# Kernel optimization log

Measured on AMD Instinct MI355X. Metric: run time of the kernel, lower is better.

Reference implementation:

```python
import jax, jax.numpy as jnp
import numpy as np

N_EMBD = 768
HEAD_SIZE = 64
B, T = 8, 4096


def setup_inputs() -> dict:
    key = jax.random.key(0)
    ks = jax.random.split(key, 7)
    s = 0.02  # small init scale for weights
    return {
        "x": jax.random.normal(ks[0], (B, T, N_EMBD), dtype=jnp.float32),
        "Wq": jax.random.normal(ks[1], (N_EMBD, HEAD_SIZE), dtype=jnp.float32) * s,
        "bq": jax.random.normal(ks[2], (HEAD_SIZE,), dtype=jnp.float32) * s,
        "Wk": jax.random.normal(ks[3], (N_EMBD, HEAD_SIZE), dtype=jnp.float32) * s,
        "bk": jax.random.normal(ks[4], (HEAD_SIZE,), dtype=jnp.float32) * s,
        "Wv": jax.random.normal(ks[5], (N_EMBD, HEAD_SIZE), dtype=jnp.float32) * s,
        "bv": jax.random.normal(ks[6], (HEAD_SIZE,), dtype=jnp.float32) * s,
    }


def reference(x, Wq, bq, Wk, bk, Wv, bv):
    # x: [B, T, C]; note: scale uses C = n_embd (input dim), per the original code.
    C = x.shape[-1]
    scale = jnp.asarray(C, x.dtype) ** -0.5
    q = x @ Wq + bq  # [B, T, H]
    k = x @ Wk + bk  # [B, T, H]
    v = x @ Wv + bv  # [B, T, H]
    wei = jnp.einsum("bqh,bkh->bqk", q, k) * scale  # [B, T, T]
    att = jax.nn.softmax(wei, axis=-1)
    # dropout p=0.0 (eval mode) -> identity
    out = jnp.einsum("bqk,bkh->bqh", att, v)  # [B, T, H]
    return out
```

## Files before the change

### kernel.cpp

```cpp
#include <hip/hip_runtime.h>
#include <stdint.h>

#define T_SEQ 4096
#define CEMB 768
#define HS 64

typedef __attribute__((ext_vector_type(8))) short bf16x8;
typedef __attribute__((ext_vector_type(16))) float f32x16;
typedef __attribute__((ext_vector_type(4))) unsigned int u32x4;

__device__ __forceinline__ short bfru(float f) {
    uint32_t u = __builtin_bit_cast(uint32_t, f);
    return (short)((u + 0x8000u) >> 16);
}
__device__ __forceinline__ uint32_t cvtpk_bf16(float lo, float hi) {
    uint32_t r;
    asm("v_cvt_pk_bf16_f32 %0, %1, %2" : "=v"(r) : "v"(lo), "v"(hi));
    return r;
}

#define QSCALE (0.036084391824351615f * 1.4426950408889634f)

__global__ __launch_bounds__(256) void prep_wt(const float* __restrict__ Wq,
                                               const float* __restrict__ Wk,
                                               const float* __restrict__ Wv,
                                               short* __restrict__ wtf) {
    const int p = blockIdx.x;
    const int tid = threadIdx.x;
    const int lane = tid & 63, jp = tid >> 6;
    const int l31 = lane & 31, lhi = lane >> 5;
    const int kq = p % 48, ct = p / 48;
    const int k = kq * 16 + lhi * 8 + jp * 2;
    const int nn = ct * 32 + l31;
    const float* W = nn < 64 ? Wq : (nn < 128 ? Wk : Wv);
    const int col = nn & 63;
    uint32_t lo = (uint16_t)bfru(W[k * 64 + col]);
    uint32_t hi = (uint16_t)bfru(W[(k + 1) * 64 + col]);
    *(uint32_t*)&wtf[(p * 64 + lane) * 8 + jp * 2] = lo | (hi << 16);
}

__global__ __launch_bounds__(256, 4) void qkv_proj(const float* __restrict__ x,
        const float* __restrict__ bq, const float* __restrict__ bk, const float* __restrict__ bv,
        const short* __restrict__ wtf,
        short* __restrict__ qo, short* __restrict__ ko, short* __restrict__ vto) {
    __shared__ short S[2][32 * 72];

    const int tid  = threadIdx.x;
    const int wave = tid >> 6, lane = tid & 63;
    const int l31  = lane & 31, lhi = lane >> 5;
    const int rowbase = blockIdx.x * 32;
    const int ctA  = wave;
    const bool hasB = (wave < 2);
    const int ctB  = wave + 4;

    f32x16 acc0, acc1;
    {
        const int nnA = ctA * 32 + l31;
        const float bA = nnA < 64 ? bq[nnA] : bk[nnA - 64];
        float bB = 0.f;
        if (hasB) bB = bv[(ctB - 4) * 32 + l31];
        #pragma unroll
        for (int r = 0; r < 16; ++r) { acc0[r] = bA; acc1[r] = bB; }
    }

    const int sr = tid >> 3, sseg = (tid & 7) * 8;
    const float* xrow = x + (long)(rowbase + sr) * CEMB + sseg;
    const short* wfA = wtf + (long)ctA * 48 * 512 + lane * 8;
    const short* wfB = wtf + (long)ctB * 48 * 512 + lane * 8;

    float4 RA0, RA1, RB0, RB1;
    {
        const float4* s0 = (const float4*)xrow;
        RA0 = s0[0]; RA1 = s0[1];
        const float4* s1 = (const float4*)(xrow + 64);
        RB0 = s1[0]; RB1 = s1[1];
        bf16x8 w;
        w[0]=bfru(RA0.x); w[1]=bfru(RA0.y); w[2]=bfru(RA0.z); w[3]=bfru(RA0.w);
        w[4]=bfru(RA1.x); w[5]=bfru(RA1.y); w[6]=bfru(RA1.z); w[7]=bfru(RA1.w);
        *(bf16x8*)&S[0][sr * 72 + sseg] = w;
    }
    __syncthreads();

    #pragma unroll
    for (int kt = 0; kt < 12; ++kt) {
        const int cur = kt & 1;
        bf16x8 wA[4], wB[4];
        #pragma unroll
        for (int kc = 0; kc < 4; ++kc)
            wA[kc] = *(const bf16x8*)(wfA + ((kt * 4 + kc) << 9));
        if (hasB) {
            #pragma unroll
            for (int kc = 0; kc < 4; ++kc)
                wB[kc] = *(const bf16x8*)(wfB + ((kt * 4 + kc) << 9));
        }
        if (kt + 2 < 12) {
            const float4* sn = (const float4*)(xrow + (kt + 2) * 64);
            if (cur == 0) { RA0 = sn[0]; RA1 = sn[1]; }
            else          { RB0 = sn[0]; RB1 = sn[1]; }
        }
        #pragma unroll
        for (int kc = 0; kc < 4; ++kc) {
            bf16x8 af = *(const bf16x8*)&S[cur][l31 * 72 + kc * 16 + lhi * 8];
            acc0 = __builtin_amdgcn_mfma_f32_32x32x16_bf16(af, wA[kc], acc0, 0, 0, 0);
            if (hasB)
                acc1 = __builtin_amdgcn_mfma_f32_32x32x16_bf16(af, wB[kc], acc1, 0, 0, 0);
        }
        if (kt + 1 < 12) {
            bf16x8 w;
            if (cur == 0) {
                w[0]=bfru(RB0.x); w[1]=bfru(RB0.y); w[2]=bfru(RB0.z); w[3]=bfru(RB0.w);
                w[4]=bfru(RB1.x); w[5]=bfru(RB1.y); w[6]=bfru(RB1.z); w[7]=bfru(RB1.w);
            } else {
                w[0]=bfru(RA0.x); w[1]=bfru(RA0.y); w[2]=bfru(RA0.z); w[3]=bfru(RA0.w);
                w[4]=bfru(RA1.x); w[5]=bfru(RA1.y); w[6]=bfru(RA1.z); w[7]=bfru(RA1.w);
            }
            *(bf16x8*)&S[cur ^ 1][sr * 72 + sseg] = w;
        }
        __syncthreads();
    }

    if (ctA < 2) {
        #pragma unroll
        for (int r = 0; r < 16; ++r) {
            const int row = (r & 3) + 8 * (r >> 2) + 4 * lhi;
            qo[(long)(rowbase + row) * HS + ctA * 32 + l31] = bfru(acc0[r] * QSCALE);
        }
    } else {
        #pragma unroll
        for (int r = 0; r < 16; ++r) {
            const int row = (r & 3) + 8 * (r >> 2) + 4 * lhi;
            ko[(long)(rowbase + row) * HS + (ctA - 2) * 32 + l31] = bfru(acc0[r]);
        }
    }
    short* Sf = (short*)S;
    if (hasB) {
        #pragma unroll
        for (int r = 0; r < 16; ++r) {
            const int row = (r & 3) + 8 * (r >> 2) + 4 * lhi;
            Sf[((ctB - 4) * 32 + l31) * 40 + row] = bfru(acc1[r]);
        }
    }
    __syncthreads();
    {
        const int vcol = tid >> 2, tseg = (tid & 3) * 8;
        const int b = rowbase >> 12, t0 = rowbase & 4095;
        *(bf16x8*)(vto + ((long)b * HS + vcol) * T_SEQ + t0 + tseg)
            = *(const bf16x8*)&Sf[vcol * 40 + tseg];
    }
}

__global__ __launch_bounds__(256, 2) void attn(const short* __restrict__ qm,
        const short* __restrict__ km, const short* __restrict__ vtm,
        float* __restrict__ Op, float* __restrict__ lp, const int ks,
        float* __restrict__ outdirect) {
    __shared__ short Klds[2][64 * 72];
    __shared__ short Vlds[2][64 * 72];
    __shared__ float Lred[4][2][32];

    const int tid  = threadIdx.x;
    const int wave = tid >> 6, lane = tid & 63;
    const int l31  = lane & 31, lhi = lane >> 5;
    const int idx  = blockIdx.x;
    const int b = idx & 7, s = (idx >> 3) % ks, qt = idx / (8 * ks);
    const int slab = T_SEQ / ks, nkt = slab / 64;

    const short* qb = qm + ((long)b * T_SEQ + qt * 256 + wave * 64) * HS;
    const short* kb = km + ((long)b * T_SEQ + s * slab) * HS;
    const short* vb = vtm + (long)b * HS * T_SEQ + s * slab;

    bf16x8 qf[2][4];
    #pragma unroll
    for (int qs = 0; qs < 2; ++qs)
        #pragma unroll
        for (int kc = 0; kc < 4; ++kc)
            qf[qs][kc] = *(const bf16x8*)&qb[(qs * 32 + l31) * HS + kc * 16 + lhi * 8];

    f32x16 oacc[2][2] = {};
    float lsum[2] = {0.f, 0.f};

    const int sr = tid >> 2, sc = (tid & 3) * 16;
    const short* kp = kb + sr * HS + sc;
    const short* vp = vb + sr * T_SEQ + sc;

    bf16x8 kr0 = *(const bf16x8*)kp, kr1 = *(const bf16x8*)(kp + 8);
    bf16x8 vr0 = *(const bf16x8*)vp, vr1 = *(const bf16x8*)(vp + 8);
    *(bf16x8*)&Klds[0][sr * 72 + sc]     = kr0;
    *(bf16x8*)&Klds[0][sr * 72 + sc + 8] = kr1;
    *(bf16x8*)&Vlds[0][sr * 72 + sc]     = vr0;
    *(bf16x8*)&Vlds[0][sr * 72 + sc + 8] = vr1;
    __syncthreads();

    for (int kt = 0; kt < nkt; ++kt) {
        const int cur = kt & 1;
        const bool pfe = (kt + 1 < nkt);
        if (pfe) {
            const short* kp2 = kp + (kt + 1) * (64 * HS);
            const short* vp2 = vp + (kt + 1) * 64;
            kr0 = *(const bf16x8*)kp2; kr1 = *(const bf16x8*)(kp2 + 8);
            vr0 = *(const bf16x8*)vp2; vr1 = *(const bf16x8*)(vp2 + 8);
        }
        const short* Kc = Klds[cur];
        const short* Vc = Vlds[cur];
        #pragma unroll
        for (int ct = 0; ct < 2; ++ct) {
            const short* krow = &Kc[(ct * 32 + l31) * 72 + lhi * 8];
            bf16x8 kf0 = *(const bf16x8*)(krow);
            bf16x8 kf1 = *(const bf16x8*)(krow + 16);
            bf16x8 kf2 = *(const bf16x8*)(krow + 32);
            bf16x8 kf3 = *(const bf16x8*)(krow + 48);
            const short* vrow = &Vc[l31 * 72 + ct * 32 + lhi * 8];
            bf16x8 vf00 = *(const bf16x8*)(vrow);
            bf16x8 vf10 = *(const bf16x8*)(vrow + 16);
            bf16x8 vf01 = *(const bf16x8*)(vrow + 32 * 72);
            bf16x8 vf11 = *(const bf16x8*)(vrow + 32 * 72 + 16);
            #pragma unroll
            for (int qs = 0; qs < 2; ++qs) {
                f32x16 z = {};
                z = __builtin_amdgcn_mfma_f32_32x32x16_bf16(kf0, qf[qs][0], z, 0, 0, 0);
                z = __builtin_amdgcn_mfma_f32_32x32x16_bf16(kf1, qf[qs][1], z, 0, 0, 0);
                z = __builtin_amdgcn_mfma_f32_32x32x16_bf16(kf2, qf[qs][2], z, 0, 0, 0);
                z = __builtin_amdgcn_mfma_f32_32x32x16_bf16(kf3, qf[qs][3], z, 0, 0, 0);
                #pragma unroll
                for (int r = 0; r < 16; ++r) z[r] = __builtin_amdgcn_exp2f(z[r]);
                lsum[qs] += (((z[0]+z[1])+(z[2]+z[3])) + ((z[4]+z[5])+(z[6]+z[7])))
                          + (((z[8]+z[9])+(z[10]+z[11])) + ((z[12]+z[13])+(z[14]+z[15])));
                uint32_t x0 = cvtpk_bf16(z[0],  z[1]),  y0 = cvtpk_bf16(z[4],  z[5]);
                uint32_t x1 = cvtpk_bf16(z[2],  z[3]),  y1 = cvtpk_bf16(z[6],  z[7]);
                uint32_t x2 = cvtpk_bf16(z[8],  z[9]),  y2 = cvtpk_bf16(z[12], z[13]);
                uint32_t x3 = cvtpk_bf16(z[10], z[11]), y3 = cvtpk_bf16(z[14], z[15]);
                asm("v_permlane32_swap_b32 %0, %1" : "+v"(x0), "+v"(y0));
                asm("v_permlane32_swap_b32 %0, %1" : "+v"(x1), "+v"(y1));
                asm("v_permlane32_swap_b32 %0, %1" : "+v"(x2), "+v"(y2));
                asm("v_permlane32_swap_b32 %0, %1" : "+v"(x3), "+v"(y3));
                u32x4 t0 = {x0, x1, y0, y1};
                u32x4 t1 = {x2, x3, y2, y3};
                bf16x8 pa0 = __builtin_bit_cast(bf16x8, t0);
                bf16x8 pa1 = __builtin_bit_cast(bf16x8, t1);
                oacc[qs][0] = __builtin_amdgcn_mfma_f32_32x32x16_bf16(pa0, vf00, oacc[qs][0], 0, 0, 0);
                oacc[qs][1] = __builtin_amdgcn_mfma_f32_32x32x16_bf16(pa0, vf01, oacc[qs][1], 0, 0, 0);
                oacc[qs][0] = __builtin_amdgcn_mfma_f32_32x32x16_bf16(pa1, vf10, oacc[qs][0], 0, 0, 0);
                oacc[qs][1] = __builtin_amdgcn_mfma_f32_32x32x16_bf16(pa1, vf11, oacc[qs][1], 0, 0, 0);
            }
        }
        if (pfe) {
            short* Kn = (short*)Klds[cur ^ 1];
            short* Vn = (short*)Vlds[cur ^ 1];
            *(bf16x8*)&Kn[sr * 72 + sc]     = kr0;
            *(bf16x8*)&Kn[sr * 72 + sc + 8] = kr1;
            *(bf16x8*)&Vn[sr * 72 + sc]     = vr0;
            *(bf16x8*)&Vn[sr * 72 + sc + 8] = vr1;
        }
        __syncthreads();
    }

    #pragma unroll
    for (int qs = 0; qs < 2; ++qs) lsum[qs] += __shfl_xor(lsum[qs], 32);

    const long rowg = (long)b * T_SEQ + qt * 256 + wave * 64;
    if (outdirect) {
        if (lhi == 0) { Lred[wave][0][l31] = lsum[0]; Lred[wave][1][l31] = lsum[1]; }
        __syncthreads();
        float* ob = outdirect + rowg * HS;
        #pragma unroll
        for (int qs = 0; qs < 2; ++qs)
            #pragma unroll
            for (int ht = 0; ht < 2; ++ht)
                #pragma unroll
                for (int r = 0; r < 16; ++r) {
                    const int row = (r & 3) + 8 * (r >> 2) + 4 * lhi;
                    ob[(long)(qs * 32 + row) * HS + ht * 32 + l31] =
                        oacc[qs][ht][r] / Lred[wave][qs][row];
                }
    } else {
        float* op = Op + ((long)s * 32768 + rowg) * HS;
        #pragma unroll
        for (int qs = 0; qs < 2; ++qs)
            #pragma unroll
            for (int ht = 0; ht < 2; ++ht)
                #pragma unroll
                for (int r = 0; r < 16; ++r) {
                    const int row = (r & 3) + 8 * (r >> 2) + 4 * lhi;
                    op[(qs * 32 + row) * HS + ht * 32 + l31] = oacc[qs][ht][r];
                }
        if (lhi == 0) {
            lp[(long)s * 32768 + rowg + l31]      = lsum[0];
            lp[(long)s * 32768 + rowg + 32 + l31] = lsum[1];
        }
    }
}

__global__ __launch_bounds__(256) void combine(const float4* __restrict__ Op,
        const float* __restrict__ lp, float4* __restrict__ out, const int ks) {
    const int idx = blockIdx.x * 256 + threadIdx.x;
    const int row = idx >> 4, h4 = idx & 15;
    float ox = 0.f, oy = 0.f, oz = 0.f, ow = 0.f, l = 0.f;
    for (int s = 0; s < ks; ++s) {
        float4 t = Op[(long)(s * 32768 + row) * 16 + h4];
        ox += t.x; oy += t.y; oz += t.z; ow += t.w;
        l += lp[s * 32768 + row];
    }
    const float inv = 1.0f / l;
    float4 o; o.x = ox * inv; o.y = oy * inv; o.z = oz * inv; o.w = ow * inv;
    out[(long)row * 16 + h4] = o;
}

extern "C" void kernel_launch(void* const* d_in, const int* in_sizes, int n_in,
                              void* d_out, int out_size, void* d_ws, size_t ws_size,
                              hipStream_t stream) {
    const float* x  = (const float*)d_in[0];
    const float* Wq = (const float*)d_in[1];
    const float* bq = (const float*)d_in[2];
    const float* Wk = (const float*)d_in[3];
    const float* bk = (const float*)d_in[4];
    const float* Wv = (const float*)d_in[5];
    const float* bv = (const float*)d_in[6];

    char* ws = (char*)d_ws;
    short* qo  = (short*)(ws);
    short* ko  = (short*)(ws + (4u << 20));
    short* vto = (short*)(ws + (8u << 20));
    short* wtf = (short*)(ws + (12u << 20));
    const size_t opOff = 12582912u + 294912u;
    float* Op = (float*)(ws + opOff);

    const size_t per_s = 8388608u + 131072u;
    int ks = (ws_size >= opOff + 4 * per_s) ? 4
           : (ws_size >= opOff + 2 * per_s) ? 2 : 1;
    float* lp = (float*)(ws + opOff + (size_t)ks * 8388608u);

    prep_wt<<<288, 256, 0, stream>>>(Wq, Wk, Wv, wtf);
    qkv_proj<<<1024, 256, 0, stream>>>(x, bq, bk, bv, wtf, qo, ko, vto);
    attn<<<128 * ks, 256, 0, stream>>>(qo, ko, vto, Op, lp, ks,
                                       ks == 1 ? (float*)d_out : nullptr);
    if (ks > 1)
        combine<<<2048, 256, 0, stream>>>((const float4*)Op, lp, (float4*)d_out, ks);
}
```

Baseline: 213.8 us.

## Halve per-wave query rows in attention to raise occupancy and block count

Each wave now handles 32 query rows instead of 64, so a block covers 128 queries and the grid doubles. Launch bounds go from 2 to 4 blocks per CU, since fewer accumulator and Q-fragment registers are needed. This trades occupancy and latency hiding against K/V reuse: each K/V tile loaded into LDS now feeds half as many queries, so global and LDS traffic per FLOP doubles.

```diff
diff --git a/kernel.cpp b/kernel.cpp
--- a/kernel.cpp
+++ b/kernel.cpp
@@ -149,13 +149,13 @@
     }
 }
 
-__global__ __launch_bounds__(256, 2) void attn(const short* __restrict__ qm,
+__global__ __launch_bounds__(256, 4) void attn(const short* __restrict__ qm,
         const short* __restrict__ km, const short* __restrict__ vtm,
         float* __restrict__ Op, float* __restrict__ lp, const int ks,
         float* __restrict__ outdirect) {
     __shared__ short Klds[2][64 * 72];
     __shared__ short Vlds[2][64 * 72];
-    __shared__ float Lred[4][2][32];
+    __shared__ float Lred[4][32];
 
     const int tid  = threadIdx.x;
     const int wave = tid >> 6, lane = tid & 63;
@@ -164,19 +164,17 @@
     const int b = idx & 7, s = (idx >> 3) % ks, qt = idx / (8 * ks);
     const int slab = T_SEQ / ks, nkt = slab / 64;
 
-    const short* qb = qm + ((long)b * T_SEQ + qt * 256 + wave * 64) * HS;
+    const short* qb = qm + ((long)b * T_SEQ + qt * 128 + wave * 32) * HS;
     const short* kb = km + ((long)b * T_SEQ + s * slab) * HS;
     const short* vb = vtm + (long)b * HS * T_SEQ + s * slab;
 
-    bf16x8 qf[2][4];
+    bf16x8 qf[4];
     #pragma unroll
-    for (int qs = 0; qs < 2; ++qs)
-        #pragma unroll
-        for (int kc = 0; kc < 4; ++kc)
-            qf[qs][kc] = *(const bf16x8*)&qb[(qs * 32 + l31) * HS + kc * 16 + lhi * 8];
-
-    f32x16 oacc[2][2] = {};
-    float lsum[2] = {0.f, 0.f};
+    for (int kc = 0; kc < 4; ++kc)
+        qf[kc] = *(const bf16x8*)&qb[l31 * HS + kc * 16 + lhi * 8];
+
+    f32x16 oacc[2] = {};
+    float lsum = 0.f;
 
     const int sr = tid >> 2, sc = (tid & 3) * 16;
     const short* kp = kb + sr * HS + sc;
@@ -213,34 +211,32 @@
             bf16x8 vf10 = *(const bf16x8*)(vrow + 16);
             bf16x8 vf01 = *(const bf16x8*)(vrow + 32 * 72);
             bf16x8 vf11 = *(const bf16x8*)(vrow + 32 * 72 + 16);
+
+            f32x16 z = {};
+            z = __builtin_amdgcn_mfma_f32_32x32x16_bf16(kf0, qf[0], z, 0, 0, 0);
+            z = __builtin_amdgcn_mfma_f32_32x32x16_bf16(kf1, qf[1], z, 0, 0, 0);
+            z = __builtin_amdgcn_mfma_f32_32x32x16_bf16(kf2, qf[2], z, 0, 0, 0);
+            z = __builtin_amdgcn_mfma_f32_32x32x16_bf16(kf3, qf[3], z, 0, 0, 0);
             #pragma unroll
-            for (int qs = 0; qs < 2; ++qs) {
-                f32x16 z = {};
-                z = __builtin_amdgcn_mfma_f32_32x32x16_bf16(kf0, qf[qs][0], z, 0, 0, 0);
-                z = __builtin_amdgcn_mfma_f32_32x32x16_bf16(kf1, qf[qs][1], z, 0, 0, 0);
-                z = __builtin_amdgcn_mfma_f32_32x32x16_bf16(kf2, qf[qs][2], z, 0, 0, 0);
-                z = __builtin_amdgcn_mfma_f32_32x32x16_bf16(kf3, qf[qs][3], z, 0, 0, 0);
-                #pragma unroll
-                for (int r = 0; r < 16; ++r) z[r] = __builtin_amdgcn_exp2f(z[r]);
-                lsum[qs] += (((z[0]+z[1])+(z[2]+z[3])) + ((z[4]+z[5])+(z[6]+z[7])))
-                          + (((z[8]+z[9])+(z[10]+z[11])) + ((z[12]+z[13])+(z[14]+z[15])));
-                uint32_t x0 = cvtpk_bf16(z[0],  z[1]),  y0 = cvtpk_bf16(z[4],  z[5]);
-                uint32_t x1 = cvtpk_bf16(z[2],  z[3]),  y1 = cvtpk_bf16(z[6],  z[7]);
-                uint32_t x2 = cvtpk_bf16(z[8],  z[9]),  y2 = cvtpk_bf16(z[12], z[13]);
-                uint32_t x3 = cvtpk_bf16(z[10], z[11]), y3 = cvtpk_bf16(z[14], z[15]);
-                asm("v_permlane32_swap_b32 %0, %1" : "+v"(x0), "+v"(y0));
-                asm("v_permlane32_swap_b32 %0, %1" : "+v"(x1), "+v"(y1));
-                asm("v_permlane32_swap_b32 %0, %1" : "+v"(x2), "+v"(y2));
-                asm("v_permlane32_swap_b32 %0, %1" : "+v"(x3), "+v"(y3));
-                u32x4 t0 = {x0, x1, y0, y1};
-                u32x4 t1 = {x2, x3, y2, y3};
-                bf16x8 pa0 = __builtin_bit_cast(bf16x8, t0);
-                bf16x8 pa1 = __builtin_bit_cast(bf16x8, t1);
-                oacc[qs][0] = __builtin_amdgcn_mfma_f32_32x32x16_bf16(pa0, vf00, oacc[qs][0], 0, 0, 0);
-                oacc[qs][1] = __builtin_amdgcn_mfma_f32_32x32x16_bf16(pa0, vf01, oacc[qs][1], 0, 0, 0);
-                oacc[qs][0] = __builtin_amdgcn_mfma_f32_32x32x16_bf16(pa1, vf10, oacc[qs][0], 0, 0, 0);
-                oacc[qs][1] = __builtin_amdgcn_mfma_f32_32x32x16_bf16(pa1, vf11, oacc[qs][1], 0, 0, 0);
-            }
+            for (int r = 0; r < 16; ++r) z[r] = __builtin_amdgcn_exp2f(z[r]);
+            lsum += (((z[0]+z[1])+(z[2]+z[3])) + ((z[4]+z[5])+(z[6]+z[7])))
+                  + (((z[8]+z[9])+(z[10]+z[11])) + ((z[12]+z[13])+(z[14]+z[15])));
+            uint32_t x0 = cvtpk_bf16(z[0],  z[1]),  y0 = cvtpk_bf16(z[4],  z[5]);
+            uint32_t x1 = cvtpk_bf16(z[2],  z[3]),  y1 = cvtpk_bf16(z[6],  z[7]);
+            uint32_t x2 = cvtpk_bf16(z[8],  z[9]),  y2 = cvtpk_bf16(z[12], z[13]);
+            uint32_t x3 = cvtpk_bf16(z[10], z[11]), y3 = cvtpk_bf16(z[14], z[15]);
+            asm("v_permlane32_swap_b32 %0, %1" : "+v"(x0), "+v"(y0));
+            asm("v_permlane32_swap_b32 %0, %1" : "+v"(x1), "+v"(y1));
+            asm("v_permlane32_swap_b32 %0, %1" : "+v"(x2), "+v"(y2));
+            asm("v_permlane32_swap_b32 %0, %1" : "+v"(x3), "+v"(y3));
+            u32x4 t0 = {x0, x1, y0, y1};
+            u32x4 t1 = {x2, x3, y2, y3};
+            bf16x8 pa0 = __builtin_bit_cast(bf16x8, t0);
+            bf16x8 pa1 = __builtin_bit_cast(bf16x8, t1);
+            oacc[0] = __builtin_amdgcn_mfma_f32_32x32x16_bf16(pa0, vf00, oacc[0], 0, 0, 0);
+            oacc[1] = __builtin_amdgcn_mfma_f32_32x32x16_bf16(pa0, vf01, oacc[1], 0, 0, 0);
+            oacc[0] = __builtin_amdgcn_mfma_f32_32x32x16_bf16(pa1, vf10, oacc[0], 0, 0, 0);
+            oacc[1] = __builtin_amdgcn_mfma_f32_32x32x16_bf16(pa1, vf11, oacc[1], 0, 0, 0);
         }
         if (pfe) {
             short* Kn = (short*)Klds[cur ^ 1];
@@ -253,39 +249,31 @@
         __syncthreads();
     }
 
-    #pragma unroll
-    for (int qs = 0; qs < 2; ++qs) lsum[qs] += __shfl_xor(lsum[qs], 32);
-
-    const long rowg = (long)b * T_SEQ + qt * 256 + wave * 64;
+    lsum += __shfl_xor(lsum, 32);
+
+    const long rowg = (long)b * T_SEQ + qt * 128 + wave * 32;
     if (outdirect) {
-        if (lhi == 0) { Lred[wave][0][l31] = lsum[0]; Lred[wave][1][l31] = lsum[1]; }
+        if (lhi == 0) Lred[wave][l31] = lsum;
         __syncthreads();
         float* ob = outdirect + rowg * HS;
         #pragma unroll
-        for (int qs = 0; qs < 2; ++qs)
+        for (int ht = 0; ht < 2; ++ht)
             #pragma unroll
-            for (int ht = 0; ht < 2; ++ht)
-                #pragma unroll
-                for (int r = 0; r < 16; ++r) {
-                    const int row = (r & 3) + 8 * (r >> 2) + 4 * lhi;
-                    ob[(long)(qs * 32 + row) * HS + ht * 32 + l31] =
-                        oacc[qs][ht][r] / Lred[wave][qs][row];
-                }
+            for (int r = 0; r < 16; ++r) {
+                const int row = (r & 3) + 8 * (r >> 2) + 4 * lhi;
+                ob[(long)row * HS + ht * 32 + l31] = oacc[ht][r] / Lred[wave][row];
+            }
     } else {
         float* op = Op + ((long)s * 32768 + rowg) * HS;
         #pragma unroll
-        for (int qs = 0; qs < 2; ++qs)
+        for (int ht = 0; ht < 2; ++ht)
             #pragma unroll
-            for (int ht = 0; ht < 2; ++ht)
-                #pragma unroll
-                for (int r = 0; r < 16; ++r) {
-                    const int row = (r & 3) + 8 * (r >> 2) + 4 * lhi;
-                    op[(qs * 32 + row) * HS + ht * 32 + l31] = oacc[qs][ht][r];
-                }
-        if (lhi == 0) {
-            lp[(long)s * 32768 + rowg + l31]      = lsum[0];
-            lp[(long)s * 32768 + rowg + 32 + l31] = lsum[1];
-        }
+            for (int r = 0; r < 16; ++r) {
+                const int row = (r & 3) + 8 * (r >> 2) + 4 * lhi;
+                op[row * HS + ht * 32 + l31] = oacc[ht][r];
+            }
+        if (lhi == 0)
+            lp[(long)s * 32768 + rowg + l31] = lsum;
     }
 }
 
@@ -330,7 +318,7 @@
 
     prep_wt<<<288, 256, 0, stream>>>(Wq, Wk, Wv, wtf);
     qkv_proj<<<1024, 256, 0, stream>>>(x, bq, bk, bv, wtf, qo, ko, vto);
-    attn<<<128 * ks, 256, 0, stream>>>(qo, ko, vto, Op, lp, ks,
+    attn<<<256 * ks, 256, 0, stream>>>(qo, ko, vto, Op, lp, ks,
                                        ks == 1 ? (float*)d_out : nullptr);
     if (ks > 1)
         combine<<<2048, 256, 0, stream>>>((const float4*)Op, lp, (float4*)d_out, ks);
```

New measurement: 217.3 us. No clear change (+1.6%).
